# Kernel tuning notes

Hardware: AMD Instinct MI355X
Metric: run time of the kernel (lower is better)

## Reference

```python
import jax, jax.numpy as jnp
import numpy as np

B = 1_000_000
N_DIR, N_TRIAL = 2, 4
ALPHA, R_GAS, EPS = 0.3, 8.314462618, 1e-12
TAU_CLIP, LN_CLIP = 10.0, 20.0
EPS_FD, SIGMA, MARGIN = 1e-4, 0.05, 0.0
LAM_PHY, LAM_GD, LAM_TPD = 1.0, 0.1, 0.1


def renorm3(x):
    # clamp to >=0 and normalize so components sum to 1 (last axis)
    x = jnp.maximum(x, 0.0)
    return x / jnp.maximum(x.sum(-1, keepdims=True), EPS)


def nrtl_ln_gamma(x, T, g):
    # x: (B,3), T: (B,), g: (B,3,3) -> ln_gamma: (B,3)
    x = jnp.maximum(x, 0.0)
    Tc = jnp.maximum(T, 1.0)
    tau = jnp.clip(g / (R_GAS * jnp.maximum(Tc, EPS)[:, None, None]), -TAU_CLIP, TAU_CLIP)
    G = jnp.exp(-ALPHA * tau)
    denom = jnp.maximum(jnp.einsum('bj,bji->bi', x, G), EPS)          # (B,3)
    A = jnp.einsum('bj,bji->bi', x, tau * G)                          # (B,3), == num1 in torch
    term1 = A / denom
    W = x[:, None, :] * G / denom[:, None, :]                         # (B,3,3)
    inside = tau - (A / denom)[:, None, :]
    term2 = (W * inside).sum(-1)
    return jnp.clip(term1 + term2, -LN_CLIP, LN_CLIP)


def setup_inputs() -> dict:
    key = jax.random.key(0)
    k1, k2, k3, k4, k5, k6 = jax.random.split(key, 6)
    pred = jax.random.uniform(k1, (B, 6), dtype=jnp.float32, minval=0.01, maxval=1.0)
    target = jax.random.uniform(k2, (B, 6), dtype=jnp.float32, minval=0.01, maxval=1.0)
    T = 298.0 + 100.0 * jax.random.uniform(k3, (B,), dtype=jnp.float32)  # Kelvin
    g = 800.0 * jax.random.normal(k4, (B, 3, 3), dtype=jnp.float32)      # J/mol
    # simplex directions: zero-sum, unit-norm (matches _sample_simplex_directions)
    v = jax.random.normal(k5, (N_DIR, B, 3), dtype=jnp.float32)
    v = v - v.mean(-1, keepdims=True)
    dirs = v / jnp.maximum(jnp.linalg.norm(v, axis=-1, keepdims=True), 1e-12)
    noise = SIGMA * jax.random.normal(k6, (N_TRIAL, B, 3), dtype=jnp.float32)
    return {'pred': pred, 'target': target, 'T': T, 'g': g, 'dirs': dirs, 'noise': noise}


def reference(pred, target, T, g, dirs, noise):
    # supervised MSE on (E+R) compositions
    L_sup = jnp.mean((pred - target) ** 2)

    xE = renorm3(pred[:, :3])
    xR = renorm3(pred[:, 3:])
    ln_gE = nrtl_ln_gamma(xE, T, g)
    ln_gR = nrtl_ln_gamma(xR, T, g)
    # chemical potential residual r_k = ln(xE_k gE_k) - ln(xR_k gR_k)
    r = jnp.log(jnp.maximum(xE, EPS)) + ln_gE - (jnp.log(jnp.maximum(xR, EPS)) + ln_gR)
    L_phy = jnp.mean(r ** 2)

    lg = jax.vmap(lambda xx: nrtl_ln_gamma(xx, T, g))  # over trial/direction axis

    # Gibbs-Duhem finite-difference penalty along simplex directions
    x_p = renorm3(xE[None] + EPS_FD * dirs)            # (N_DIR,B,3)
    x_m = renorm3(xE[None] - EPS_FD * dirs)
    d_ln = (lg(x_p) - lg(x_m)) / (2.0 * EPS_FD)
    gd = (xE[None] * d_ln).sum(-1)                     # (N_DIR,B)
    L_gd = jnp.mean(gd * gd)

    # TPD stability penalty
    w = renorm3(xE[None] + noise)                      # (N_TRIAL,B,3)
    ln_gw = lg(w)
    tpd = (w * (jnp.log(jnp.maximum(w, EPS)) + ln_gw
                - jnp.log(jnp.maximum(xE, EPS))[None] - ln_gE[None])).sum(-1)
    L_tpd = jnp.mean(jnp.maximum(MARGIN - tpd, 0.0))

    return L_sup + LAM_PHY * L_phy + LAM_GD * L_gd + LAM_TPD * L_tpd
```

## Files before the change

### kernel.cpp

```cpp
#include <hip/hip_runtime.h>


constexpr float ALPHA    = 0.3f;
constexpr float R_GAS    = 8.314462618f;
constexpr float EPS      = 1e-12f;
constexpr float TAU_CLIP = 10.0f;
constexpr float LN_CLIP  = 20.0f;
constexpr float EPS_FD   = 1e-4f;

constexpr float LOG2E = 1.44269504088896340736f;
constexpr float LN2   = 0.69314718055994530942f;

typedef float v2f __attribute__((ext_vector_type(2)));

__device__ __forceinline__ float clipf(float v, float lo, float hi) {
    return fminf(fmaxf(v, lo), hi);
}
__device__ __forceinline__ float fast_rcp(float x) { return __builtin_amdgcn_rcpf(x); }
__device__ __forceinline__ v2f nt_load2(const float* p) {
    return __builtin_nontemporal_load((const v2f*)p);
}
__device__ __forceinline__ float nt_load(const float* p) {
    return __builtin_nontemporal_load(p);
}

struct Mats {
    float tau[3][3];
    float G[3][3];
    float tG[3][3];
};

__device__ __forceinline__ void ln_gamma3(const float x[3], const Mats& M, float lg[3]) {
    float ratio[3], invd[3];
#pragma unroll
    for (int i = 0; i < 3; ++i) {
        float d = x[0] * M.G[0][i] + x[1] * M.G[1][i] + x[2] * M.G[2][i];
        d = fmaxf(d, EPS);
        float A = x[0] * M.tG[0][i] + x[1] * M.tG[1][i] + x[2] * M.tG[2][i];
        float inv = fast_rcp(d);
        invd[i] = inv;
        ratio[i] = A * inv;
    }
#pragma unroll
    for (int i = 0; i < 3; ++i) {
        float s = ratio[i];
#pragma unroll
        for (int j = 0; j < 3; ++j) {
            s += x[j] * M.G[i][j] * invd[j] * (M.tau[i][j] - ratio[j]);
        }
        lg[i] = clipf(s, -LN_CLIP, LN_CLIP);
    }
}

__device__ __forceinline__ void renorm3(float x[3]) {
    x[0] = fmaxf(x[0], 0.0f);
    x[1] = fmaxf(x[1], 0.0f);
    x[2] = fmaxf(x[2], 0.0f);
    float inv = fast_rcp(fmaxf(x[0] + x[1] + x[2], EPS));
    x[0] *= inv; x[1] *= inv; x[2] *= inv;
}

__global__ __launch_bounds__(256) void nrtl_loss_kernel(
    const float* __restrict__ pred,
    const float* __restrict__ target,
    const float* __restrict__ Tarr,
    const float* __restrict__ g,
    const float* __restrict__ dirs,
    const float* __restrict__ noise,
    float* __restrict__ partials, int B)
{
    const int i = blockIdx.x * blockDim.x + threadIdx.x;
    float contrib = 0.0f;

    if (i < B) {
        const float* prow = pred   + (size_t)i * 6;
        const float* trow = target + (size_t)i * 6;
        const float* grow = g      + (size_t)i * 9;

        v2f p01 = nt_load2(prow);
        v2f p23 = nt_load2(prow + 2);
        v2f p45 = nt_load2(prow + 4);
        v2f t01 = nt_load2(trow);
        v2f t23 = nt_load2(trow + 2);
        v2f t45 = nt_load2(trow + 4);

        float sup;
        {
            float d0 = p01.x - t01.x, d1 = p01.y - t01.y;
            float d2 = p23.x - t23.x, d3 = p23.y - t23.y;
            float d4 = p45.x - t45.x, d5 = p45.y - t45.y;
            sup = d0 * d0 + d1 * d1 + d2 * d2 + d3 * d3 + d4 * d4 + d5 * d5;
        }

        float xE[3] = {p01.x, p01.y, p23.x};
        float xR[3] = {p23.y, p45.x, p45.y};
        renorm3(xE);
        renorm3(xR);

        const float Tc = fmaxf(nt_load(Tarr + i), 1.0f);
        const float invRT = fast_rcp(R_GAS * Tc);
        Mats M;
#pragma unroll
        for (int a = 0; a < 3; ++a) {
#pragma unroll
            for (int b = 0; b < 3; ++b) {
                float ta = clipf(nt_load(grow + a * 3 + b) * invRT, -TAU_CLIP, TAU_CLIP);
                float Gv = __builtin_amdgcn_exp2f((-ALPHA * LOG2E) * ta);
                M.tau[a][b] = ta;
                M.G[a][b]   = Gv;
                M.tG[a][b]  = ta * Gv;
            }
        }

        float lgE[3], lgR[3];
        ln_gamma3(xE, M, lgE);
        ln_gamma3(xR, M, lgR);

        float logxE[3];
        float phy = 0.0f;
#pragma unroll
        for (int k = 0; k < 3; ++k) {
            logxE[k] = LN2 * __builtin_amdgcn_logf(fmaxf(xE[k], EPS));
            float logxR = LN2 * __builtin_amdgcn_logf(fmaxf(xR[k], EPS));
            float r = logxE[k] + lgE[k] - logxR - lgR[k];
            phy += r * r;
        }

        float gdsum = 0.0f;
#pragma unroll
        for (int d = 0; d < 2; ++d) {
            const float* drow = dirs + ((size_t)d * B + i) * 3;
            float dv[3];
#pragma unroll
            for (int k = 0; k < 3; ++k) dv[k] = nt_load(drow + k);
            float xp[3], xm[3];
#pragma unroll
            for (int k = 0; k < 3; ++k) {
                xp[k] = xE[k] + EPS_FD * dv[k];
                xm[k] = xE[k] - EPS_FD * dv[k];
            }
            renorm3(xp);
            renorm3(xm);
            float lgp[3], lgm[3];
            ln_gamma3(xp, M, lgp);
            ln_gamma3(xm, M, lgm);
            float gd = 0.0f;
            const float inv2e = 0.5f / EPS_FD;
#pragma unroll
            for (int k = 0; k < 3; ++k) gd += xE[k] * ((lgp[k] - lgm[k]) * inv2e);
            gdsum += gd * gd;
        }

        float tpdsum = 0.0f;
#pragma unroll
        for (int tr = 0; tr < 4; ++tr) {
            const float* nrow = noise + ((size_t)tr * B + i) * 3;
            float w[3];
#pragma unroll
            for (int k = 0; k < 3; ++k) w[k] = xE[k] + nt_load(nrow + k);
            renorm3(w);
            float lgw[3];
            ln_gamma3(w, M, lgw);
            float tpd = 0.0f;
#pragma unroll
            for (int k = 0; k < 3; ++k) {
                float logw = LN2 * __builtin_amdgcn_logf(fmaxf(w[k], EPS));
                tpd += w[k] * (logw + lgw[k] - logxE[k] - lgE[k]);
            }
            tpdsum += fmaxf(-tpd, 0.0f);
        }

        const float invB = 1.0f / (float)B;
        contrib = invB * (sup * (1.0f / 6.0f)
                          + phy * (1.0f / 3.0f)
                          + 0.05f * gdsum
                          + 0.025f * tpdsum);
    }

#pragma unroll
    for (int off = 32; off > 0; off >>= 1)
        contrib += __shfl_down(contrib, off, 64);

    __shared__ float ssum[4];
    const int lane = threadIdx.x & 63;
    const int wid  = threadIdx.x >> 6;
    if (lane == 0) ssum[wid] = contrib;
    __syncthreads();
    if (threadIdx.x == 0) {
        partials[blockIdx.x] = ssum[0] + ssum[1] + ssum[2] + ssum[3];
    }
}

__global__ __launch_bounds__(256) void reduce_kernel(
    const float* __restrict__ partials, int n, float* __restrict__ out)
{
    double sacc = 0.0;
    for (int j = threadIdx.x; j < n; j += 256) sacc += (double)partials[j];
#pragma unroll
    for (int off = 32; off > 0; off >>= 1)
        sacc += __shfl_down(sacc, off, 64);
    __shared__ double ds[4];
    const int lane = threadIdx.x & 63;
    const int wid  = threadIdx.x >> 6;
    if (lane == 0) ds[wid] = sacc;
    __syncthreads();
    if (threadIdx.x == 0) out[0] = (float)(ds[0] + ds[1] + ds[2] + ds[3]);
}

extern "C" void kernel_launch(void* const* d_in, const int* in_sizes, int n_in,
                              void* d_out, int out_size, void* d_ws, size_t ws_size,
                              hipStream_t stream) {
    const float* pred   = (const float*)d_in[0];
    const float* target = (const float*)d_in[1];
    const float* Tarr   = (const float*)d_in[2];
    const float* g      = (const float*)d_in[3];
    const float* dirs   = (const float*)d_in[4];
    const float* noise  = (const float*)d_in[5];
    const int B = in_sizes[2];

    float* partials = (float*)d_ws;
    float* out      = (float*)d_out;

    const int block = 256;
    const int grid  = (B + block - 1) / block;
    nrtl_loss_kernel<<<grid, block, 0, stream>>>(pred, target, Tarr, g, dirs, noise, partials, B);
    reduce_kernel<<<1, block, 0, stream>>>(partials, grid, out);
}
```

Before: 174.3 us.

## Hoist all per-row global loads to kernel start and simplify NRTL inner term

All loads of T, g, dirs and noise are issued at the start of the thread so their latencies overlap, instead of being interleaved with dependent compute. The ln_gamma inner sum is rewritten algebraically to use precomputed tau*G and x/denom, which cuts multiplies per term. The launch bounds now request 4 blocks per CU, and minor constant hoisting is added in the GD and TPD loops. Holding the extra loaded values in registers earlier raises register pressure, which the occupancy hint may constrain.

```diff
diff --git a/kernel.cpp b/kernel.cpp
--- a/kernel.cpp
+++ b/kernel.cpp
@@ -31,22 +31,22 @@
 };
 
 __device__ __forceinline__ void ln_gamma3(const float x[3], const Mats& M, float lg[3]) {
-    float ratio[3], invd[3];
+    float ratio[3], c[3];
 #pragma unroll
     for (int i = 0; i < 3; ++i) {
         float d = x[0] * M.G[0][i] + x[1] * M.G[1][i] + x[2] * M.G[2][i];
         d = fmaxf(d, EPS);
         float A = x[0] * M.tG[0][i] + x[1] * M.tG[1][i] + x[2] * M.tG[2][i];
         float inv = fast_rcp(d);
-        invd[i] = inv;
         ratio[i] = A * inv;
+        c[i] = x[i] * inv;
     }
 #pragma unroll
     for (int i = 0; i < 3; ++i) {
         float s = ratio[i];
 #pragma unroll
         for (int j = 0; j < 3; ++j) {
-            s += x[j] * M.G[i][j] * invd[j] * (M.tau[i][j] - ratio[j]);
+            s += c[j] * (M.tG[i][j] - M.G[i][j] * ratio[j]);
         }
         lg[i] = clipf(s, -LN_CLIP, LN_CLIP);
     }
@@ -60,7 +60,7 @@
     x[0] *= inv; x[1] *= inv; x[2] *= inv;
 }
 
-__global__ __launch_bounds__(256) void nrtl_loss_kernel(
+__global__ __launch_bounds__(256, 4) void nrtl_loss_kernel(
     const float* __restrict__ pred,
     const float* __restrict__ target,
     const float* __restrict__ Tarr,
@@ -83,6 +83,24 @@
         v2f t01 = nt_load2(trow);
         v2f t23 = nt_load2(trow + 2);
         v2f t45 = nt_load2(trow + 4);
+        float Tv = nt_load(Tarr + i);
+        float gv[9];
+#pragma unroll
+        for (int k = 0; k < 9; ++k) gv[k] = nt_load(grow + k);
+        float dv[2][3];
+#pragma unroll
+        for (int d = 0; d < 2; ++d) {
+            const float* drow = dirs + ((size_t)d * B + i) * 3;
+#pragma unroll
+            for (int k = 0; k < 3; ++k) dv[d][k] = nt_load(drow + k);
+        }
+        float nv[4][3];
+#pragma unroll
+        for (int tr = 0; tr < 4; ++tr) {
+            const float* nrow = noise + ((size_t)tr * B + i) * 3;
+#pragma unroll
+            for (int k = 0; k < 3; ++k) nv[tr][k] = nt_load(nrow + k);
+        }
 
         float sup;
         {
@@ -97,14 +115,14 @@
         renorm3(xE);
         renorm3(xR);
 
-        const float Tc = fmaxf(nt_load(Tarr + i), 1.0f);
+        const float Tc = fmaxf(Tv, 1.0f);
         const float invRT = fast_rcp(R_GAS * Tc);
         Mats M;
 #pragma unroll
         for (int a = 0; a < 3; ++a) {
 #pragma unroll
             for (int b = 0; b < 3; ++b) {
-                float ta = clipf(nt_load(grow + a * 3 + b) * invRT, -TAU_CLIP, TAU_CLIP);
+                float ta = clipf(gv[a * 3 + b] * invRT, -TAU_CLIP, TAU_CLIP);
                 float Gv = __builtin_amdgcn_exp2f((-ALPHA * LOG2E) * ta);
                 M.tau[a][b] = ta;
                 M.G[a][b]   = Gv;
@@ -129,15 +147,11 @@
         float gdsum = 0.0f;
 #pragma unroll
         for (int d = 0; d < 2; ++d) {
-            const float* drow = dirs + ((size_t)d * B + i) * 3;
-            float dv[3];
-#pragma unroll
-            for (int k = 0; k < 3; ++k) dv[k] = nt_load(drow + k);
             float xp[3], xm[3];
 #pragma unroll
             for (int k = 0; k < 3; ++k) {
-                xp[k] = xE[k] + EPS_FD * dv[k];
-                xm[k] = xE[k] - EPS_FD * dv[k];
+                xp[k] = xE[k] + EPS_FD * dv[d][k];
+                xm[k] = xE[k] - EPS_FD * dv[d][k];
             }
             renorm3(xp);
             renorm3(xm);
@@ -145,19 +159,22 @@
             ln_gamma3(xp, M, lgp);
             ln_gamma3(xm, M, lgm);
             float gd = 0.0f;
-            const float inv2e = 0.5f / EPS_FD;
-#pragma unroll
-            for (int k = 0; k < 3; ++k) gd += xE[k] * ((lgp[k] - lgm[k]) * inv2e);
+#pragma unroll
+            for (int k = 0; k < 3; ++k) gd += xE[k] * (lgp[k] - lgm[k]);
+            gd *= 0.5f / EPS_FD;
             gdsum += gd * gd;
         }
 
+        float base[3];
+#pragma unroll
+        for (int k = 0; k < 3; ++k) base[k] = logxE[k] + lgE[k];
+
         float tpdsum = 0.0f;
 #pragma unroll
         for (int tr = 0; tr < 4; ++tr) {
-            const float* nrow = noise + ((size_t)tr * B + i) * 3;
             float w[3];
 #pragma unroll
-            for (int k = 0; k < 3; ++k) w[k] = xE[k] + nt_load(nrow + k);
+            for (int k = 0; k < 3; ++k) w[k] = xE[k] + nv[tr][k];
             renorm3(w);
             float lgw[3];
             ln_gamma3(w, M, lgw);
@@ -165,7 +182,7 @@
 #pragma unroll
             for (int k = 0; k < 3; ++k) {
                 float logw = LN2 * __builtin_amdgcn_logf(fmaxf(w[k], EPS));
-                tpd += w[k] * (logw + lgw[k] - logxE[k] - lgE[k]);
+                tpd += w[k] * (logw + lgw[k] - base[k]);
             }
             tpdsum += fmaxf(-tpd, 0.0f);
         }
```

Measured after the change: 169.3 us. -2.9%, faster.

## Pack paired NRTL evaluations into float2 vectors for packed FP32 math

Applied to the files above, without the earlier changes.

Evaluates pairs of NRTL ln-gamma computations (E/R, plus/minus finite-difference points, pairs of TPD trials) in two-wide float vectors so the compiler can emit packed FP32 instructions. It also rewrites the inner ln-gamma term as c_j*(tG - G*ratio), with c_j = x_j/denom_j precomputed, which removes some multiplies. The cost is that the tau/G/tG matrices are duplicated into both lanes, which raises register pressure. Transcendental ops (rcp, log) stay scalar per lane.

```diff
diff --git a/kernel.cpp b/kernel.cpp
--- a/kernel.cpp
+++ b/kernel.cpp
@@ -13,10 +13,24 @@
 
 typedef float v2f __attribute__((ext_vector_type(2)));
 
+__device__ __forceinline__ v2f make2(float s) { return (v2f){s, s}; }
+__device__ __forceinline__ v2f pk_rcp(v2f a) {
+    return (v2f){__builtin_amdgcn_rcpf(a.x), __builtin_amdgcn_rcpf(a.y)};
+}
+__device__ __forceinline__ v2f pk_ln(v2f a) {
+    return make2(LN2) * (v2f){__builtin_amdgcn_logf(fmaxf(a.x, EPS)),
+                              __builtin_amdgcn_logf(fmaxf(a.y, EPS))};
+}
+__device__ __forceinline__ v2f pk_max(v2f a, v2f b) { return __builtin_elementwise_max(a, b); }
+__device__ __forceinline__ v2f pk_min(v2f a, v2f b) { return __builtin_elementwise_min(a, b); }
+__device__ __forceinline__ v2f pk_clip(v2f v, float lo, float hi) {
+    return pk_min(pk_max(v, make2(lo)), make2(hi));
+}
 __device__ __forceinline__ float clipf(float v, float lo, float hi) {
     return fminf(fmaxf(v, lo), hi);
 }
 __device__ __forceinline__ float fast_rcp(float x) { return __builtin_amdgcn_rcpf(x); }
+
 __device__ __forceinline__ v2f nt_load2(const float* p) {
     return __builtin_nontemporal_load((const v2f*)p);
 }
@@ -24,39 +38,39 @@
     return __builtin_nontemporal_load(p);
 }
 
-struct Mats {
-    float tau[3][3];
-    float G[3][3];
-    float tG[3][3];
+struct MatsP {
+    v2f tau[3][3];
+    v2f G[3][3];
+    v2f tG[3][3];
 };
 
-__device__ __forceinline__ void ln_gamma3(const float x[3], const Mats& M, float lg[3]) {
-    float ratio[3], invd[3];
+__device__ __forceinline__ void ln_gamma3p(const v2f x[3], const MatsP& M, v2f lg[3]) {
+    v2f ratio[3], c[3];
 #pragma unroll
     for (int i = 0; i < 3; ++i) {
-        float d = x[0] * M.G[0][i] + x[1] * M.G[1][i] + x[2] * M.G[2][i];
-        d = fmaxf(d, EPS);
-        float A = x[0] * M.tG[0][i] + x[1] * M.tG[1][i] + x[2] * M.tG[2][i];
-        float inv = fast_rcp(d);
-        invd[i] = inv;
+        v2f d = x[0] * M.G[0][i] + x[1] * M.G[1][i] + x[2] * M.G[2][i];
+        d = pk_max(d, make2(EPS));
+        v2f A = x[0] * M.tG[0][i] + x[1] * M.tG[1][i] + x[2] * M.tG[2][i];
+        v2f inv = pk_rcp(d);
         ratio[i] = A * inv;
+        c[i] = x[i] * inv;
     }
 #pragma unroll
     for (int i = 0; i < 3; ++i) {
-        float s = ratio[i];
+        v2f s = ratio[i];
 #pragma unroll
         for (int j = 0; j < 3; ++j) {
-            s += x[j] * M.G[i][j] * invd[j] * (M.tau[i][j] - ratio[j]);
-        }
-        lg[i] = clipf(s, -LN_CLIP, LN_CLIP);
-    }
-}
-
-__device__ __forceinline__ void renorm3(float x[3]) {
-    x[0] = fmaxf(x[0], 0.0f);
-    x[1] = fmaxf(x[1], 0.0f);
-    x[2] = fmaxf(x[2], 0.0f);
-    float inv = fast_rcp(fmaxf(x[0] + x[1] + x[2], EPS));
+            s += c[j] * (M.tG[i][j] - M.G[i][j] * ratio[j]);
+        }
+        lg[i] = pk_clip(s, -LN_CLIP, LN_CLIP);
+    }
+}
+
+__device__ __forceinline__ void renorm3p(v2f x[3]) {
+    x[0] = pk_max(x[0], make2(0.0f));
+    x[1] = pk_max(x[1], make2(0.0f));
+    x[2] = pk_max(x[2], make2(0.0f));
+    v2f inv = pk_rcp(pk_max(x[0] + x[1] + x[2], make2(EPS)));
     x[0] *= inv; x[1] *= inv; x[2] *= inv;
 }
 
@@ -92,37 +106,37 @@
             sup = d0 * d0 + d1 * d1 + d2 * d2 + d3 * d3 + d4 * d4 + d5 * d5;
         }
 
-        float xE[3] = {p01.x, p01.y, p23.x};
-        float xR[3] = {p23.y, p45.x, p45.y};
-        renorm3(xE);
-        renorm3(xR);
-
-        const float Tc = fmaxf(nt_load(Tarr + i), 1.0f);
+        v2f xER[3] = { (v2f){p01.x, p23.y},
+                       (v2f){p01.y, p45.x},
+                       (v2f){p23.x, p45.y} };
+        renorm3p(xER);
+        float xE[3] = {xER[0].x, xER[1].x, xER[2].x};
+
+        const float Tc    = fmaxf(nt_load(Tarr + i), 1.0f);
         const float invRT = fast_rcp(R_GAS * Tc);
-        Mats M;
+        MatsP M;
 #pragma unroll
         for (int a = 0; a < 3; ++a) {
 #pragma unroll
             for (int b = 0; b < 3; ++b) {
                 float ta = clipf(nt_load(grow + a * 3 + b) * invRT, -TAU_CLIP, TAU_CLIP);
                 float Gv = __builtin_amdgcn_exp2f((-ALPHA * LOG2E) * ta);
-                M.tau[a][b] = ta;
-                M.G[a][b]   = Gv;
-                M.tG[a][b]  = ta * Gv;
-            }
-        }
-
-        float lgE[3], lgR[3];
-        ln_gamma3(xE, M, lgE);
-        ln_gamma3(xR, M, lgR);
-
-        float logxE[3];
+                M.tau[a][b] = make2(ta);
+                M.G[a][b]   = make2(Gv);
+                M.tG[a][b]  = make2(ta * Gv);
+            }
+        }
+
+        v2f lgER[3];
+        ln_gamma3p(xER, M, lgER);
+
+        v2f basePk[3];
         float phy = 0.0f;
 #pragma unroll
         for (int k = 0; k < 3; ++k) {
-            logxE[k] = LN2 * __builtin_amdgcn_logf(fmaxf(xE[k], EPS));
-            float logxR = LN2 * __builtin_amdgcn_logf(fmaxf(xR[k], EPS));
-            float r = logxE[k] + lgE[k] - logxR - lgR[k];
+            v2f logx = pk_ln(xER[k]);
+            basePk[k] = logx + lgER[k];
+            float r = basePk[k].x - basePk[k].y;
             phy += r * r;
         }
 
@@ -130,44 +144,45 @@
 #pragma unroll
         for (int d = 0; d < 2; ++d) {
             const float* drow = dirs + ((size_t)d * B + i) * 3;
-            float dv[3];
-#pragma unroll
-            for (int k = 0; k < 3; ++k) dv[k] = nt_load(drow + k);
-            float xp[3], xm[3];
+            v2f xpm[3];
 #pragma unroll
             for (int k = 0; k < 3; ++k) {
-                xp[k] = xE[k] + EPS_FD * dv[k];
-                xm[k] = xE[k] - EPS_FD * dv[k];
-            }
-            renorm3(xp);
-            renorm3(xm);
-            float lgp[3], lgm[3];
-            ln_gamma3(xp, M, lgp);
-            ln_gamma3(xm, M, lgm);
+                float e = EPS_FD * nt_load(drow + k);
+                xpm[k] = make2(xE[k]) + (v2f){e, -e};
+            }
+            renorm3p(xpm);
+            v2f lgpm[3];
+            ln_gamma3p(xpm, M, lgpm);
             float gd = 0.0f;
-            const float inv2e = 0.5f / EPS_FD;
-#pragma unroll
-            for (int k = 0; k < 3; ++k) gd += xE[k] * ((lgp[k] - lgm[k]) * inv2e);
+#pragma unroll
+            for (int k = 0; k < 3; ++k) gd += xE[k] * (lgpm[k].x - lgpm[k].y);
+            gd *= 0.5f / EPS_FD;
             gdsum += gd * gd;
         }
 
+        v2f baseB[3];
+#pragma unroll
+        for (int k = 0; k < 3; ++k) baseB[k] = make2(basePk[k].x);
+
         float tpdsum = 0.0f;
 #pragma unroll
-        for (int tr = 0; tr < 4; ++tr) {
-            const float* nrow = noise + ((size_t)tr * B + i) * 3;
-            float w[3];
-#pragma unroll
-            for (int k = 0; k < 3; ++k) w[k] = xE[k] + nt_load(nrow + k);
-            renorm3(w);
-            float lgw[3];
-            ln_gamma3(w, M, lgw);
-            float tpd = 0.0f;
+        for (int tp = 0; tp < 2; ++tp) {
+            const float* nrA = noise + ((size_t)(2 * tp)     * B + i) * 3;
+            const float* nrB = noise + ((size_t)(2 * tp + 1) * B + i) * 3;
+            v2f w[3];
 #pragma unroll
             for (int k = 0; k < 3; ++k) {
-                float logw = LN2 * __builtin_amdgcn_logf(fmaxf(w[k], EPS));
-                tpd += w[k] * (logw + lgw[k] - logxE[k] - lgE[k]);
-            }
-            tpdsum += fmaxf(-tpd, 0.0f);
+                w[k] = (v2f){xE[k] + nt_load(nrA + k), xE[k] + nt_load(nrB + k)};
+            }
+            renorm3p(w);
+            v2f lgw[3];
+            ln_gamma3p(w, M, lgw);
+            v2f tpd = make2(0.0f);
+#pragma unroll
+            for (int k = 0; k < 3; ++k) {
+                tpd += w[k] * (pk_ln(w[k]) + lgw[k] - baseB[k]);
+            }
+            tpdsum += fmaxf(-tpd.x, 0.0f) + fmaxf(-tpd.y, 0.0f);
         }
 
         const float invB = 1.0f / (float)B;
```

After: 168.8 us. 1.03x faster.
